# Kernel optimization log

Hardware: AMD Instinct MI355X
Metric: run time of the kernel (lower is better)

## Reference

```python
import jax, jax.numpy as jnp
import numpy as np

EPS = 1e-3    # Keras BatchNormalization default epsilon
ALPHA = 0.3   # Keras LeakyReLU default negative slope


def _bn(x, axes):
    # BatchNormalization(center=False, scale=False) in training mode: batch stats
    m = jnp.mean(x, axis=axes, keepdims=True)
    v = jnp.var(x, axis=axes, keepdims=True)
    return (x - m) * jax.lax.rsqrt(v + EPS)


def _leaky(x):
    return jnp.where(x > 0, x, ALPHA * x)


def setup_inputs() -> dict:
    key = jax.random.key(0)
    ks = jax.random.split(key, 8)
    B, A, D, Hid, H, hd = 8192, 16, 256, 512, 8, 64
    s = 0.02
    return {
        "state": jax.random.normal(ks[0], (B, A, D), jnp.float32),
        "agent_index": 3,
        "Ws": jax.random.normal(ks[1], (D, Hid), jnp.float32) * s,
        "bs": jnp.zeros((Hid,), jnp.float32),
        "Wc": jax.random.normal(ks[2], (D, Hid), jnp.float32) * s,
        "bc": jnp.zeros((Hid,), jnp.float32),
        "Wk": jax.random.normal(ks[3], (H, Hid, hd), jnp.float32) * s,
        "Wq": jax.random.normal(ks[4], (H, Hid, hd), jnp.float32) * s,
        "Wv": jax.random.normal(ks[5], (H, Hid, hd), jnp.float32) * s,
    }


def reference(state, agent_index, Ws, bs, Wc, bc, Wk, Wq, Wv):
    B = state.shape[0]
    H, _, hd = Wk.shape
    ai = int(agent_index)

    # current agent encoder: BN over batch, Dense, LeakyReLU -> [B, Hid]
    cur = state[:, ai, :]
    s_enc = _leaky(_bn(cur, (0,)) @ Ws + bs)

    # other agents encoder: BN over (batch, agent), Dense, LeakyReLU -> [B, A-1, Hid]
    others = jnp.concatenate([state[:, :ai, :], state[:, ai + 1:, :]], axis=1)
    sa_enc = _leaky(_bn(others, (0, 1)) @ Wc + bc)

    # batched per-head projections (replaces the python loop over heads)
    k = jnp.einsum('ban,hnd->bhad', sa_enc, Wk)           # [B,H,A-1,hd]
    v = _leaky(jnp.einsum('ban,hnd->bhad', sa_enc, Wv))   # [B,H,A-1,hd]
    q = jnp.einsum('bn,hnd->bhd', s_enc, Wq)              # [B,H,hd]

    scores = jnp.einsum('bhd,bhad->bha', q, k) / jnp.sqrt(jnp.float32(hd))
    w = jax.nn.softmax(scores, axis=-1)                   # [B,H,A-1]
    att = jnp.einsum('bha,bhad->bhd', w, v)               # [B,H,hd]

    # concat heads in order -> [B, H*hd]
    return att.reshape(B, H * hd)
```

## Files before the change

kernel.cpp:

```cpp
#include <hip/hip_runtime.h>
#include <hip/hip_bf16.h>

typedef __attribute__((ext_vector_type(8))) short short8;
typedef __attribute__((ext_vector_type(8))) unsigned short ushort8;
typedef __attribute__((ext_vector_type(4))) unsigned short bfu4;
typedef __attribute__((ext_vector_type(4))) float f32x4;

__device__ __forceinline__ unsigned short f2bf(float f){
  return __builtin_bit_cast(unsigned short, __float2bfloat16(f));
}
__device__ __forceinline__ float bf2f(unsigned short h){
  unsigned int u = ((unsigned int)h) << 16;
  return __builtin_bit_cast(float, u);
}
__device__ __forceinline__ float leaky(float x){ return x > 0.f ? x : 0.3f * x; }

__global__ __launch_bounds__(1024) void ca_stats_partial(const float* __restrict__ state,
    const int* __restrict__ agp, float* __restrict__ part, int B){
  int q = threadIdx.x & 63, sl = threadIdx.x >> 6;
  int ag = agp[0];
  int bPer = (B + 255) >> 8;
  int b0 = blockIdx.x * bPer;
  f32x4 zero4 = {0.f,0.f,0.f,0.f};
  f32x4 sC = zero4, ssC = zero4, sO = zero4, ssO = zero4;
  for (int b = sl; b < bPer; b += 16){
    int bb = b0 + b;
    if (bb >= B) continue;
    const float* row = state + ((size_t)bb << 12) + q*4;
    #pragma unroll
    for (int a = 0; a < 16; a++){
      f32x4 v = *(const f32x4*)(row + a*256);
      f32x4 vv = v * v;
      if (a == ag){ sC += v; ssC += vv; } else { sO += v; ssO += vv; }
    }
  }
  __shared__ f32x4 red[16][4][64];
  red[sl][0][q] = sC; red[sl][1][q] = ssC; red[sl][2][q] = sO; red[sl][3][q] = ssO;
  __syncthreads();
  if (threadIdx.x < 256){
    int st = threadIdx.x >> 6, qq = threadIdx.x & 63;
    f32x4 s = red[0][st][qq];
    #pragma unroll
    for (int g = 1; g < 16; g++) s += red[g][st][qq];
    *(f32x4*)(part + (size_t)blockIdx.x*1024 + st*256 + qq*4) = s;
  }
}

__global__ __launch_bounds__(1024) void ca_stats_final(const float* __restrict__ part,
    float* __restrict__ stats, int nblk, int B){
  int d = threadIdx.x & 255, sl = threadIdx.x >> 8;
  float sC = 0.f, ssC = 0.f, sO = 0.f, ssO = 0.f;
  for (int g = sl; g < nblk; g += 4){
    const float* p = part + (size_t)g * 1024;
    sC += p[d]; ssC += p[d+256]; sO += p[d+512]; ssO += p[d+768];
  }
  __shared__ float red[4][4][256];
  red[sl][0][d] = sC; red[sl][1][d] = ssC; red[sl][2][d] = sO; red[sl][3][d] = ssO;
  __syncthreads();
  if (sl == 0){
    sC  = red[0][0][d] + red[1][0][d] + red[2][0][d] + red[3][0][d];
    ssC = red[0][1][d] + red[1][1][d] + red[2][1][d] + red[3][1][d];
    sO  = red[0][2][d] + red[1][2][d] + red[2][2][d] + red[3][2][d];
    ssO = red[0][3][d] + red[1][3][d] + red[2][3][d] + red[3][3][d];
    float nC = (float)B, nO = (float)B * 15.f;
    float mC = sC / nC, vC = ssC / nC - mC * mC;
    float mO = sO / nO, vO = ssO / nO - mO * mO;
    float rC = rsqrtf(vC + 1e-3f), rO = rsqrtf(vO + 1e-3f);
    stats[d] = rC; stats[d+256] = mC * rC; stats[d+512] = rO; stats[d+768] = mO * rO;
  }
}

__global__ __launch_bounds__(256) void ca_prep_sc(const float* __restrict__ Ws,
    const float* __restrict__ bs, const float* __restrict__ Wc, const float* __restrict__ bc,
    const float* __restrict__ stats, unsigned short* __restrict__ WsT,
    unsigned short* __restrict__ WcT, unsigned short* __restrict__ WsF,
    unsigned short* __restrict__ WcF, float* __restrict__ bsp, float* __restrict__ bcp,
    int writeT){
  int n = blockIdx.x, d = threadIdx.x;
  float rC = stats[d], mrC = stats[d+256], rO = stats[d+512], mrO = stats[d+768];
  float ws = Ws[(size_t)d*512 + n], wc = Wc[(size_t)d*512 + n];
  unsigned short wsb = f2bf(ws * rC), wcb = f2bf(wc * rO);
  if (writeT){
    WsT[(size_t)n*256 + d] = wsb;
    WcT[(size_t)n*256 + d] = wcb;
  }
  {
    int h = n >> 6, nt = (n >> 4) & 3, j = n & 15;
    int kk = d >> 5, hi = (d >> 3) & 3, e = d & 7;
    size_t fi = (size_t)((h*8 + kk)*4 + nt)*512 + (hi*16 + j)*8 + e;
    WsF[fi] = wsb;
    WcF[fi] = wcb;
  }
  __shared__ float red[256];
  red[d] = mrC * ws;
  __syncthreads();
  for (int s = 128; s > 0; s >>= 1){ if (d < s) red[d] += red[d+s]; __syncthreads(); }
  if (d == 0) bsp[n] = bs[n] - red[0];
  __syncthreads();
  red[d] = mrO * wc;
  __syncthreads();
  for (int s = 128; s > 0; s >>= 1){ if (d < s) red[d] += red[d+s]; __syncthreads(); }
  if (d == 0) bcp[n] = bc[n] - red[0];
}

__global__ __launch_bounds__(512) void ca_prep_kvq(const float* __restrict__ Wk,
    const float* __restrict__ Wv, const float* __restrict__ Wq,
    unsigned short* __restrict__ WkT, unsigned short* __restrict__ WvT,
    unsigned short* __restrict__ WqT, unsigned short* __restrict__ WkF2,
    unsigned short* __restrict__ WvF, unsigned short* __restrict__ WqF, int writeT){
  int c = blockIdx.x & 511, m = blockIdx.x >> 9;
  int n = threadIdx.x;
  if (m == 3){
    size_t idx = (size_t)c*512 + n;
    int h = (int)(idx >> 15), nn = (int)((idx >> 6) & 511), dd = (int)(idx & 63);
    int nt = nn >> 4, j = nn & 15, kq = dd >> 5, hi = (dd >> 3) & 3, e = dd & 7;
    WkF2[(size_t)((h*32 + nt)*2 + kq)*512 + (hi*16 + j)*8 + e] = f2bf(Wk[idx]);
    return;
  }
  if (m == 0 && !writeT) return;
  int h = c >> 6, dd = c & 63;
  const float* W = (m == 0) ? Wk : (m == 1) ? Wv : Wq;
  unsigned short* O = (m == 0) ? WkT : (m == 1) ? WvT : WqT;
  float scale = (m == 2) ? 0.125f : 1.f;
  unsigned short v = f2bf(W[((size_t)h*512 + n)*64 + dd] * scale);
  if (m == 0 || writeT) O[(size_t)c*512 + n] = v;
  if (m != 0){
    int nt = (c >> 4) & 3, j = c & 15;
    int kk = n >> 5, hi = (n >> 3) & 3, e = n & 7;
    size_t fi = (size_t)((h*16 + kk)*4 + nt)*512 + (hi*16 + j)*8 + e;
    if (m == 1) WvF[fi] = v; else WqF[fi] = v;
  }
}

__global__ __launch_bounds__(512) void ca_q_kernel(const float* __restrict__ state,
    const int* __restrict__ agp,
    const unsigned short* __restrict__ WsT, const float* __restrict__ bsp,
    const unsigned short* __restrict__ WqT, unsigned short* __restrict__ Qws){
  __shared__ unsigned short U[32*512];
  __shared__ float bias_s[512];
  unsigned short* Alds = U;
  unsigned short* SE = U;
  int tid = threadIdx.x, lane = tid & 63, w = tid >> 6;
  int j = lane & 15, hi = lane >> 4;
  int b0 = blockIdx.x * 32;
  int ag = agp[0];

  for (int s = tid; s < 32*32; s += 512){
    int row = s >> 5, kg = s & 31;
    const float* p = state + (((size_t)(b0 + row) * 16 + ag) << 8) + kg * 8;
    f32x4 v0 = *(const f32x4*)p, v1 = *(const f32x4*)(p + 4);
    ushort8 hv;
    hv[0]=f2bf(v0[0]); hv[1]=f2bf(v0[1]); hv[2]=f2bf(v0[2]); hv[3]=f2bf(v0[3]);
    hv[4]=f2bf(v1[0]); hv[5]=f2bf(v1[1]); hv[6]=f2bf(v1[2]); hv[7]=f2bf(v1[3]);
    *(ushort8*)&Alds[row*256 + ((kg ^ (row & 7)) << 3)] = hv;
  }
  bias_s[tid & 511] = bsp[tid & 511];
  __syncthreads();

  int cb = w * 64;
  f32x4 zero4 = {0.f, 0.f, 0.f, 0.f};
  f32x4 acc[2][4];
  #pragma unroll
  for (int a1 = 0; a1 < 2; a1++)
    #pragma unroll
    for (int a2 = 0; a2 < 4; a2++) acc[a1][a2] = zero4;

  #pragma unroll
  for (int kk = 0; kk < 8; kk++){
    short8 bfr[4];
    #pragma unroll
    for (int nt = 0; nt < 4; nt++)
      bfr[nt] = *(const short8*)&WsT[(size_t)(cb + nt*16 + j)*256 + kk*32 + hi*8];
    #pragma unroll
    for (int mt = 0; mt < 2; mt++){
      int row = mt*16 + j;
      short8 afr = *(const short8*)&Alds[row*256 + ((((kk << 2) | hi) ^ (row & 7)) << 3)];
      #pragma unroll
      for (int nt = 0; nt < 4; nt++)
        acc[mt][nt] = __builtin_amdgcn_mfma_f32_16x16x32_bf16(afr, bfr[nt], acc[mt][nt], 0, 0, 0);
    }
  }
  __syncthreads();
  #pragma unroll
  for (int mt = 0; mt < 2; mt++)
    #pragma unroll
    for (int nt = 0; nt < 4; nt++)
      #pragma unroll
      for (int i = 0; i < 4; i++){
        int row = mt*16 + hi*4 + i, col = cb + nt*16 + j;
        float x = leaky(acc[mt][nt][i] + bias_s[col]);
        SE[row*512 + ((((col >> 3) ^ (row & 7)) << 3) | (col & 7))] = f2bf(x);
      }
  __syncthreads();

  f32x4 qa[2][4];
  #pragma unroll
  for (int a1 = 0; a1 < 2; a1++)
    #pragma unroll
    for (int a2 = 0; a2 < 4; a2++) qa[a1][a2] = zero4;
  #pragma unroll
  for (int kk = 0; kk < 16; kk++){
    short8 bfr[4];
    #pragma unroll
    for (int nt = 0; nt < 4; nt++)
      bfr[nt] = *(const short8*)&WqT[(size_t)(cb + nt*16 + j)*512 + kk*32 + hi*8];
    #pragma unroll
    for (int mt = 0; mt < 2; mt++){
      int row = mt*16 + j;
      short8 afr = *(const short8*)&SE[row*512 + ((((kk << 2) | hi) ^ (row & 7)) << 3)];
      #pragma unroll
      for (int nt = 0; nt < 4; nt++)
        qa[mt][nt] = __builtin_amdgcn_mfma_f32_16x16x32_bf16(afr, bfr[nt], qa[mt][nt], 0, 0, 0);
    }
  }
  #pragma unroll
  for (int mt = 0; mt < 2; mt++)
    #pragma unroll
    for (int nt = 0; nt < 4; nt++)
      #pragma unroll
      for (int i = 0; i < 4; i++)
        Qws[(size_t)(b0 + mt*16 + hi*4 + i)*512 + cb + nt*16 + j] = f2bf(qa[mt][nt][i]);
}

__global__ __launch_bounds__(512) void ca_q_kernel_qk(const float* __restrict__ state,
    const int* __restrict__ agp,
    const unsigned short* __restrict__ WsF, const float* __restrict__ bsp,
    const unsigned short* __restrict__ WqF, const unsigned short* __restrict__ WkF2,
    unsigned short* __restrict__ QKws){
  __shared__ unsigned short U[16*512];
  __shared__ float bias_s[512];
  unsigned short* Alds = U;
  unsigned short* SE = U;
  unsigned short* Qlds = U;
  int tid = threadIdx.x, lane = tid & 63, w = tid >> 6;
  int j = lane & 15, hi = lane >> 4;
  int b0 = blockIdx.x * 16;
  int ag = agp[0];
  f32x4 zero4 = {0.f, 0.f, 0.f, 0.f};

  {
    int row = tid >> 5, kg = tid & 31;
    const float* p = state + (((size_t)(b0 + row) * 16 + ag) << 8) + kg * 8;
    f32x4 v0 = *(const f32x4*)p, v1 = *(const f32x4*)(p + 4);
    ushort8 hv;
    hv[0]=f2bf(v0[0]); hv[1]=f2bf(v0[1]); hv[2]=f2bf(v0[2]); hv[3]=f2bf(v0[3]);
    hv[4]=f2bf(v1[0]); hv[5]=f2bf(v1[1]); hv[6]=f2bf(v1[2]); hv[7]=f2bf(v1[3]);
    *(ushort8*)&Alds[row*256 + ((kg ^ (row & 7)) << 3)] = hv;
  }
  bias_s[tid] = bsp[tid];
  __syncthreads();

  int cb = w * 64;

  f32x4 acc[4];
  #pragma unroll
  for (int a2 = 0; a2 < 4; a2++) acc[a2] = zero4;
  #pragma unroll
  for (int kk = 0; kk < 8; kk++){
    short8 bfr[4];
    #pragma unroll
    for (int nt = 0; nt < 4; nt++)
      bfr[nt] = *(const short8*)&WsF[(size_t)((w*8 + kk)*4 + nt)*512 + lane*8];
    short8 afr = *(const short8*)&Alds[j*256 + ((((kk << 2) | hi) ^ (j & 7)) << 3)];
    #pragma unroll
    for (int nt = 0; nt < 4; nt++)
      acc[nt] = __builtin_amdgcn_mfma_f32_16x16x32_bf16(bfr[nt], afr, acc[nt], 0, 0, 0);
  }
  __syncthreads();
  #pragma unroll
  for (int nt = 0; nt < 4; nt++){
    int nb = cb + nt*16 + hi*4;
    int g = nb >> 3;
    bfu4 pk;
    #pragma unroll
    for (int i = 0; i < 4; i++) pk[i] = f2bf(leaky(acc[nt][i] + bias_s[nb + i]));
    *(bfu4*)&SE[j*512 + ((g ^ (j & 7)) << 3) + (hi & 1)*4] = pk;
  }
  __syncthreads();

  f32x4 qa[4];
  #pragma unroll
  for (int a2 = 0; a2 < 4; a2++) qa[a2] = zero4;
  #pragma unroll
  for (int kk = 0; kk < 16; kk++){
    short8 bfr[4];
    #pragma unroll
    for (int nt = 0; nt < 4; nt++)
      bfr[nt] = *(const short8*)&WqF[(size_t)((w*16 + kk)*4 + nt)*512 + lane*8];
    short8 afr = *(const short8*)&SE[j*512 + ((((kk << 2) | hi) ^ (j & 7)) << 3)];
    #pragma unroll
    for (int nt = 0; nt < 4; nt++)
      qa[nt] = __builtin_amdgcn_mfma_f32_16x16x32_bf16(bfr[nt], afr, qa[nt], 0, 0, 0);
  }
  __syncthreads();
  #pragma unroll
  for (int nt = 0; nt < 4; nt++){
    int nb = cb + nt*16 + hi*4;
    int g = nb >> 3;
    bfu4 pk;
    #pragma unroll
    for (int i = 0; i < 4; i++) pk[i] = f2bf(qa[nt][i]);
    *(bfu4*)&Qlds[j*512 + ((g ^ (j & 7)) << 3) + (hi & 1)*4] = pk;
  }
  __syncthreads();

  short8 aq[2];
  #pragma unroll
  for (int kq = 0; kq < 2; kq++){
    int gq = w*8 + kq*4 + hi;
    aq[kq] = *(const short8*)&Qlds[j*512 + ((gq ^ (j & 7)) << 3)];
  }
  for (int nt = 0; nt < 32; nt++){
    short8 bf0 = *(const short8*)&WkF2[(size_t)((w*32 + nt)*2 + 0)*512 + lane*8];
    short8 bf1 = *(const short8*)&WkF2[(size_t)((w*32 + nt)*2 + 1)*512 + lane*8];
    f32x4 qt = zero4;
    qt = __builtin_amdgcn_mfma_f32_16x16x32_bf16(bf0, aq[0], qt, 0, 0, 0);
    qt = __builtin_amdgcn_mfma_f32_16x16x32_bf16(bf1, aq[1], qt, 0, 0, 0);
    bfu4 pk;
    pk[0] = f2bf(qt[0]); pk[1] = f2bf(qt[1]); pk[2] = f2bf(qt[2]); pk[3] = f2bf(qt[3]);
    *(bfu4*)&QKws[((size_t)(b0 + j)*8 + w)*512 + nt*16 + hi*4] = pk;
  }
}

__global__ __launch_bounds__(512) void ca_main_kernel_qk(const float* __restrict__ state,
    const int* __restrict__ agp,
    const unsigned short* __restrict__ WcF, const float* __restrict__ bcp,
    const unsigned short* __restrict__ WvF, const unsigned short* __restrict__ QKws,
    float* __restrict__ out){
  __shared__ unsigned short U[128*512];
  __shared__ float bias_s[512];
  __shared__ float Wl[8*16*8];
  unsigned short* Alds = U;
  unsigned short* SA = U;
  int tid = threadIdx.x, lane = tid & 63, w = tid >> 6;
  int j = lane & 15, hi = lane >> 4;
  int b0 = blockIdx.x * 8;
  int ag = agp[0];
  f32x4 zero4 = {0.f, 0.f, 0.f, 0.f};
  short8 zero8 = {0,0,0,0,0,0,0,0};

  #pragma unroll
  for (int g = 0; g < 2; g++){
    f32x4 st0[4], st1[4];
    #pragma unroll
    for (int it = 0; it < 4; it++){
      int s = tid + 512*(g*4 + it);
      int row = s >> 5, kg = s & 31;
      int bl = row >> 4, ai = row & 15;
      if (ai < 15){
        int a = ai + (ai >= ag ? 1 : 0);
        const float* p = state + (((size_t)(b0 + bl) * 16 + a) << 8) + kg * 8;
        st0[it] = *(const f32x4*)p;
        st1[it] = *(const f32x4*)(p + 4);
      } else { st0[it] = zero4; st1[it] = zero4; }
    }
    #pragma unroll
    for (int it = 0; it < 4; it++){
      int s = tid + 512*(g*4 + it);
      int row = s >> 5, kg = s & 31;
      ushort8 hv;
      hv[0]=f2bf(st0[it][0]); hv[1]=f2bf(st0[it][1]); hv[2]=f2bf(st0[it][2]); hv[3]=f2bf(st0[it][3]);
      hv[4]=f2bf(st1[it][0]); hv[5]=f2bf(st1[it][1]); hv[6]=f2bf(st1[it][2]); hv[7]=f2bf(st1[it][3]);
      *(ushort8*)&Alds[row*256 + ((kg ^ (row & 7)) << 3)] = hv;
    }
  }
  bias_s[tid] = bcp[tid];
  __syncthreads();

  int cb = w * 64;

  f32x4 acc[8][4];
  #pragma unroll
  for (int a1 = 0; a1 < 8; a1++)
    #pragma unroll
    for (int a2 = 0; a2 < 4; a2++) acc[a1][a2] = zero4;
  {
    short8 bcur[4], bnxt[4];
    #pragma unroll
    for (int nt = 0; nt < 4; nt++)
      bcur[nt] = *(const short8*)&WcF[(size_t)((w*8 + 0)*4 + nt)*512 + lane*8];
    #pragma unroll 1
    for (int kk = 0; kk < 8; kk++){
      if (kk < 7){
        #pragma unroll
        for (int nt = 0; nt < 4; nt++)
          bnxt[nt] = *(const short8*)&WcF[(size_t)((w*8 + kk + 1)*4 + nt)*512 + lane*8];
      }
      #pragma unroll
      for (int mt = 0; mt < 8; mt++){
        int row = mt*16 + j;
        short8 afr = *(const short8*)&Alds[row*256 + ((((kk << 2) | hi) ^ (row & 7)) << 3)];
        #pragma unroll
        for (int nt = 0; nt < 4; nt++)
          acc[mt][nt] = __builtin_amdgcn_mfma_f32_16x16x32_bf16(bcur[nt], afr, acc[mt][nt], 0, 0, 0);
      }
      #pragma unroll
      for (int nt = 0; nt < 4; nt++) bcur[nt] = bnxt[nt];
    }
  }
  __syncthreads();
  #pragma unroll
  for (int mt = 0; mt < 8; mt++)
    #pragma unroll
    for (int nt = 0; nt < 4; nt++){
      int m = mt*16 + j;
      int nb = cb + nt*16 + hi*4;
      int g = nb >> 3;
      bfu4 pk;
      #pragma unroll
      for (int i = 0; i < 4; i++) pk[i] = f2bf(leaky(acc[mt][nt][i] + bias_s[nb + i]));
      *(bfu4*)&SA[m*512 + ((g ^ (m & 7)) << 3) + (hi & 1)*4] = pk;
    }
  __syncthreads();

  f32x4 qs = zero4;
  {
    size_t qbase = ((size_t)(b0 + w)*8 + (j & 7))*512;
    #pragma unroll
    for (int kk = 0; kk < 16; kk++){
      short8 bq = *(const short8*)&QKws[qbase + kk*32 + hi*8];
      if (j >= 8) bq = zero8;
      int row = w*16 + j;
      short8 afr = *(const short8*)&SA[row*512 + ((((kk << 2) | hi) ^ (row & 7)) << 3)];
      qs = __builtin_amdgcn_mfma_f32_16x16x32_bf16(afr, bq, qs, 0, 0, 0);
    }
  }
  {
    float sv0 = qs[0], sv1 = qs[1], sv2 = qs[2], sv3 = qs[3];
    sv3 = (hi == 3) ? -1e30f : sv3;
    float m = fmaxf(fmaxf(sv0, sv1), fmaxf(sv2, sv3));
    m = fmaxf(m, __shfl_xor(m, 16)); m = fmaxf(m, __shfl_xor(m, 32));
    float e0 = __expf(sv0-m), e1 = __expf(sv1-m), e2 = __expf(sv2-m), e3 = __expf(sv3-m);
    float sum = e0 + e1 + e2 + e3;
    sum += __shfl_xor(sum, 16); sum += __shfl_xor(sum, 32);
    float inv = 1.f / sum;
    if (j < 8){
      Wl[w*128 + (hi*4+0)*8 + j] = e0*inv;
      Wl[w*128 + (hi*4+1)*8 + j] = e1*inv;
      Wl[w*128 + (hi*4+2)*8 + j] = e2*inv;
      Wl[w*128 + (hi*4+3)*8 + j] = e3*inv;
    }
  }

  f32x4 va[8][4];
  #pragma unroll
  for (int a1 = 0; a1 < 8; a1++)
    #pragma unroll
    for (int a2 = 0; a2 < 4; a2++) va[a1][a2] = zero4;
  {
    short8 bcur[4], bnxt[4];
    #pragma unroll
    for (int nt = 0; nt < 4; nt++)
      bcur[nt] = *(const short8*)&WvF[(size_t)((w*16 + 0)*4 + nt)*512 + lane*8];
    #pragma unroll 1
    for (int kk = 0; kk < 16; kk++){
      if (kk < 15){
        #pragma unroll
        for (int nt = 0; nt < 4; nt++)
          bnxt[nt] = *(const short8*)&WvF[(size_t)((w*16 + kk + 1)*4 + nt)*512 + lane*8];
      }
      #pragma unroll
      for (int mt = 0; mt < 8; mt++){
        int row = mt*16 + j;
        short8 afr = *(const short8*)&SA[row*512 + ((((kk << 2) | hi) ^ (row & 7)) << 3)];
        #pragma unroll
        for (int nt = 0; nt < 4; nt++)
          va[mt][nt] = __builtin_amdgcn_mfma_f32_16x16x32_bf16(afr, bcur[nt], va[mt][nt], 0, 0, 0);
      }
      #pragma unroll
      for (int nt = 0; nt < 4; nt++) bcur[nt] = bnxt[nt];
    }
  }
  __syncthreads();

  #pragma unroll
  for (int mt = 0; mt < 8; mt++){
    float w0 = Wl[mt*128 + (hi*4+0)*8 + w];
    float w1 = Wl[mt*128 + (hi*4+1)*8 + w];
    float w2 = Wl[mt*128 + (hi*4+2)*8 + w];
    float w3 = Wl[mt*128 + (hi*4+3)*8 + w];
    float ap0 = w0*leaky(va[mt][0][0]) + w1*leaky(va[mt][0][1]) + w2*leaky(va[mt][0][2]) + w3*leaky(va[mt][0][3]);
    float ap1 = w0*leaky(va[mt][1][0]) + w1*leaky(va[mt][1][1]) + w2*leaky(va[mt][1][2]) + w3*leaky(va[mt][1][3]);
    float ap2 = w0*leaky(va[mt][2][0]) + w1*leaky(va[mt][2][1]) + w2*leaky(va[mt][2][2]) + w3*leaky(va[mt][2][3]);
    float ap3 = w0*leaky(va[mt][3][0]) + w1*leaky(va[mt][3][1]) + w2*leaky(va[mt][3][2]) + w3*leaky(va[mt][3][3]);
    ap0 += __shfl_xor(ap0, 16); ap0 += __shfl_xor(ap0, 32);
    ap1 += __shfl_xor(ap1, 16); ap1 += __shfl_xor(ap1, 32);
    ap2 += __shfl_xor(ap2, 16); ap2 += __shfl_xor(ap2, 32);
    ap3 += __shfl_xor(ap3, 16); ap3 += __shfl_xor(ap3, 32);
    float val = (hi == 0) ? ap0 : (hi == 1) ? ap1 : (hi == 2) ? ap2 : ap3;
    out[(size_t)(b0 + mt)*512 + cb + lane] = val;
  }
}

__global__ __launch_bounds__(512) void ca_main_kernel(const float* __restrict__ state,
    const int* __restrict__ agp,
    const unsigned short* __restrict__ WcT, const float* __restrict__ bcp,
    const unsigned short* __restrict__ WkT, const unsigned short* __restrict__ WvT,
    const unsigned short* __restrict__ Qws, float* __restrict__ out){
  __shared__ unsigned short U[128*512];
  __shared__ unsigned short Qs[8*512];
  __shared__ float bias_s[512];
  unsigned short* Alds = U;
  unsigned short* SA = U;
  int tid = threadIdx.x, lane = tid & 63, w = tid >> 6;
  int j = lane & 15, hi = lane >> 4;
  int b0 = blockIdx.x * 8;
  int ag = agp[0];
  f32x4 zero4 = {0.f, 0.f, 0.f, 0.f};

  #pragma unroll
  for (int g = 0; g < 2; g++){
    f32x4 st0[4], st1[4];
    #pragma unroll
    for (int it = 0; it < 4; it++){
      int s = tid + 512*(g*4 + it);
      int row = s >> 5, kg = s & 31;
      int bl = row >> 4, ai = row & 15;
      if (ai < 15){
        int a = ai + (ai >= ag ? 1 : 0);
        const float* p = state + (((size_t)(b0 + bl) * 16 + a) << 8) + kg * 8;
        st0[it] = *(const f32x4*)p;
        st1[it] = *(const f32x4*)(p + 4);
      } else { st0[it] = zero4; st1[it] = zero4; }
    }
    #pragma unroll
    for (int it = 0; it < 4; it++){
      int s = tid + 512*(g*4 + it);
      int row = s >> 5, kg = s & 31;
      ushort8 hv;
      hv[0]=f2bf(st0[it][0]); hv[1]=f2bf(st0[it][1]); hv[2]=f2bf(st0[it][2]); hv[3]=f2bf(st0[it][3]);
      hv[4]=f2bf(st1[it][0]); hv[5]=f2bf(st1[it][1]); hv[6]=f2bf(st1[it][2]); hv[7]=f2bf(st1[it][3]);
      *(ushort8*)&Alds[row*256 + ((kg ^ (row & 7)) << 3)] = hv;
    }
  }
  *(ushort8*)&Qs[tid*8] = *(const ushort8*)&Qws[(size_t)b0*512 + tid*8];
  bias_s[tid] = bcp[tid];
  __syncthreads();

  int cb = w * 64;

  f32x4 acc[8][4];
  #pragma unroll
  for (int a1 = 0; a1 < 8; a1++)
    #pragma unroll
    for (int a2 = 0; a2 < 4; a2++) acc[a1][a2] = zero4;
  {
    short8 bcur[4], bnxt[4];
    #pragma unroll
    for (int nt = 0; nt < 4; nt++)
      bcur[nt] = *(const short8*)&WcT[(size_t)(cb + nt*16 + j)*256 + hi*8];
    #pragma unroll 1
    for (int kk = 0; kk < 8; kk++){
      if (kk < 7){
        #pragma unroll
        for (int nt = 0; nt < 4; nt++)
          bnxt[nt] = *(const short8*)&WcT[(size_t)(cb + nt*16 + j)*256 + (kk+1)*32 + hi*8];
      }
      #pragma unroll
      for (int mt = 0; mt < 8; mt++){
        int row = mt*16 + j;
        short8 afr = *(const short8*)&Alds[row*256 + ((((kk << 2) | hi) ^ (row & 7)) << 3)];
        #pragma unroll
        for (int nt = 0; nt < 4; nt++)
          acc[mt][nt] = __builtin_amdgcn_mfma_f32_16x16x32_bf16(afr, bcur[nt], acc[mt][nt], 0, 0, 0);
      }
      #pragma unroll
      for (int nt = 0; nt < 4; nt++) bcur[nt] = bnxt[nt];
    }
  }
  __syncthreads();
  #pragma unroll
  for (int mt = 0; mt < 8; mt++)
    #pragma unroll
    for (int nt = 0; nt < 4; nt++)
      #pragma unroll
      for (int i = 0; i < 4; i++){
        int row = mt*16 + hi*4 + i, col = cb + nt*16 + j;
        float x = leaky(acc[mt][nt][i] + bias_s[col]);
        SA[row*512 + ((((col >> 3) ^ (row & 7)) << 3) | (col & 7))] = f2bf(x);
      }
  __syncthreads();

  f32x4 ka[8][4];
  #pragma unroll
  for (int a1 = 0; a1 < 8; a1++)
    #pragma unroll
    for (int a2 = 0; a2 < 4; a2++) ka[a1][a2] = zero4;
  {
    short8 bcur[4], bnxt[4];
    #pragma unroll
    for (int nt = 0; nt < 4; nt++)
      bcur[nt] = *(const short8*)&WkT[(size_t)(cb + nt*16 + j)*512 + hi*8];
    #pragma unroll 1
    for (int kk = 0; kk < 16; kk++){
      if (kk < 15){
        #pragma unroll
        for (int nt = 0; nt < 4; nt++)
          bnxt[nt] = *(const short8*)&WkT[(size_t)(cb + nt*16 + j)*512 + (kk+1)*32 + hi*8];
      }
      #pragma unroll
      for (int mt = 0; mt < 8; mt++){
        int row = mt*16 + j;
        short8 afr = *(const short8*)&SA[row*512 + ((((kk << 2) | hi) ^ (row & 7)) << 3)];
        #pragma unroll
        for (int nt = 0; nt < 4; nt++)
          ka[mt][nt] = __builtin_amdgcn_mfma_f32_16x16x32_bf16(afr, bcur[nt], ka[mt][nt], 0, 0, 0);
      }
      #pragma unroll
      for (int nt = 0; nt < 4; nt++) bcur[nt] = bnxt[nt];
    }
  }

  float wgt[8][4];
  #pragma unroll
  for (int mt = 0; mt < 8; mt++){
    float sv[4];
    #pragma unroll
    for (int i = 0; i < 4; i++){
      float t = 0.f;
      #pragma unroll
      for (int nt = 0; nt < 4; nt++)
        t += bf2f(Qs[mt*512 + cb + nt*16 + j]) * ka[mt][nt][i];
      t += __shfl_xor(t, 1); t += __shfl_xor(t, 2);
      t += __shfl_xor(t, 4); t += __shfl_xor(t, 8);
      sv[i] = t;
    }
    sv[3] = (hi == 3) ? -1e30f : sv[3];
    float m = fmaxf(fmaxf(sv[0], sv[1]), fmaxf(sv[2], sv[3]));
    m = fmaxf(m, __shfl_xor(m, 16)); m = fmaxf(m, __shfl_xor(m, 32));
    float e0 = __expf(sv[0]-m), e1 = __expf(sv[1]-m), e2 = __expf(sv[2]-m), e3 = __expf(sv[3]-m);
    float sum = e0 + e1 + e2 + e3;
    sum += __shfl_xor(sum, 16); sum += __shfl_xor(sum, 32);
    float inv = 1.f / sum;
    wgt[mt][0] = e0*inv; wgt[mt][1] = e1*inv; wgt[mt][2] = e2*inv; wgt[mt][3] = e3*inv;
  }

  f32x4 va[8][4];
  #pragma unroll
  for (int a1 = 0; a1 < 8; a1++)
    #pragma unroll
    for (int a2 = 0; a2 < 4; a2++) va[a1][a2] = zero4;
  {
    short8 bcur[4], bnxt[4];
    #pragma unroll
    for (int nt = 0; nt < 4; nt++)
      bcur[nt] = *(const short8*)&WvT[(size_t)(cb + nt*16 + j)*512 + hi*8];
    #pragma unroll 1
    for (int kk = 0; kk < 16; kk++){
      if (kk < 15){
        #pragma unroll
        for (int nt = 0; nt < 4; nt++)
          bnxt[nt] = *(const short8*)&WvT[(size_t)(cb + nt*16 + j)*512 + (kk+1)*32 + hi*8];
      }
      #pragma unroll
      for (int mt = 0; mt < 8; mt++){
        int row = mt*16 + j;
        short8 afr = *(const short8*)&SA[row*512 + ((((kk << 2) | hi) ^ (row & 7)) << 3)];
        #pragma unroll
        for (int nt = 0; nt < 4; nt++)
          va[mt][nt] = __builtin_amdgcn_mfma_f32_16x16x32_bf16(afr, bcur[nt], va[mt][nt], 0, 0, 0);
      }
      #pragma unroll
      for (int nt = 0; nt < 4; nt++) bcur[nt] = bnxt[nt];
    }
  }

  #pragma unroll
  for (int mt = 0; mt < 8; mt++){
    float ap0 = 0.f, ap1 = 0.f, ap2 = 0.f, ap3 = 0.f;
    #pragma unroll
    for (int i = 0; i < 4; i++){
      float wv = wgt[mt][i];
      ap0 += wv * leaky(va[mt][0][i]);
      ap1 += wv * leaky(va[mt][1][i]);
      ap2 += wv * leaky(va[mt][2][i]);
      ap3 += wv * leaky(va[mt][3][i]);
    }
    ap0 += __shfl_xor(ap0, 16); ap0 += __shfl_xor(ap0, 32);
    ap1 += __shfl_xor(ap1, 16); ap1 += __shfl_xor(ap1, 32);
    ap2 += __shfl_xor(ap2, 16); ap2 += __shfl_xor(ap2, 32);
    ap3 += __shfl_xor(ap3, 16); ap3 += __shfl_xor(ap3, 32);
    float val = (hi == 0) ? ap0 : (hi == 1) ? ap1 : (hi == 2) ? ap2 : ap3;
    out[(size_t)(b0 + mt)*512 + cb + lane] = val;
  }
}

extern "C" void kernel_launch(void* const* d_in, const int* in_sizes, int n_in,
                              void* d_out, int out_size, void* d_ws, size_t ws_size,
                              hipStream_t stream) {
  const float* state = (const float*)d_in[0];
  const int*   agp   = (const int*)d_in[1];
  const float* Ws    = (const float*)d_in[2];
  const float* bs    = (const float*)d_in[3];
  const float* Wc    = (const float*)d_in[4];
  const float* bc    = (const float*)d_in[5];
  const float* Wk    = (const float*)d_in[6];
  const float* Wq    = (const float*)d_in[7];
  const float* Wv    = (const float*)d_in[8];
  float* out = (float*)d_out;
  int B = in_sizes[0] / 4096;

  char* wsb = (char*)d_ws;
  float* part  = (float*)wsb;
  float* stats = (float*)(wsb + (1 << 20));
  float* bsp   = (float*)(wsb + (1 << 20) + 4096);
  float* bcp   = (float*)(wsb + (1 << 20) + 6144);
  unsigned short* WsT  = (unsigned short*)(wsb + (1 << 20) + 8192);
  unsigned short* WcT  = WsT  + 512*256;
  unsigned short* WkT  = WcT  + 512*256;
  unsigned short* WvT  = WkT  + 512*512;
  unsigned short* WqT  = WvT  + 512*512;
  unsigned short* WkF2 = WqT  + 512*512;
  unsigned short* Qws  = WkF2 + 512*512;
  unsigned short* QKws = Qws  + (size_t)B*512;
  unsigned short* WsF  = Qws;
  unsigned short* WcF  = WsF + 512*256;
  unsigned short* WqF  = WcF + 512*256;
  unsigned short* WvF  = WqF + 512*512;

  size_t need = ((size_t)(1 << 20) + 8192)
              + 2ull*(512*256 + 512*256 + 512*512 + 512*512 + 512*512 + 512*512)
              + 2ull*B*512 + 2ull*B*8*512;
  bool qkp = (ws_size >= need);
  int writeT = qkp ? 0 : 1;

  hipLaunchKernelGGL(ca_stats_partial, dim3(256), dim3(1024), 0, stream, state, agp, part, B);
  hipLaunchKernelGGL(ca_stats_final,   dim3(1),   dim3(1024), 0, stream, part, stats, 256, B);
  hipLaunchKernelGGL(ca_prep_sc,       dim3(512), dim3(256), 0, stream, Ws, bs, Wc, bc, stats, WsT, WcT, WsF, WcF, bsp, bcp, writeT);
  hipLaunchKernelGGL(ca_prep_kvq,      dim3(2048),dim3(512), 0, stream, Wk, Wv, Wq, WkT, WvT, WqT, WkF2, WvF, WqF, writeT);
  if (qkp){
    hipLaunchKernelGGL(ca_q_kernel_qk,   dim3(B/16),dim3(512), 0, stream, state, agp, WsF, bsp, WqF, WkF2, QKws);
    hipLaunchKernelGGL(ca_main_kernel_qk,dim3(B/8), dim3(512), 0, stream, state, agp, WcF, bcp, WvF, QKws, out);
  } else {
    hipLaunchKernelGGL(ca_q_kernel,      dim3(B/32),dim3(512), 0, stream, state, agp, WsT, bsp, WqT, Qws);
    hipLaunchKernelGGL(ca_main_kernel,   dim3(B/8), dim3(512), 0, stream, state, agp, WcT, bcp, WkT, WvT, Qws, out);
  }
}
```

Baseline: 235.6 us.

## Fuse query/QK projection into main attention kernel and parallelize stats finalization

Removes the separate ca_q_kernel_qk launch and computes the current-agent encoding, Q projection and Q·Wk products inside ca_main_kernel_qk for each block's 8 batch rows. Rows are padded to 16 with zeros, so half the MFMA work in that phase is wasted. It also splits ca_stats_final across 4 blocks of 64 features each instead of one block. This saves a launch and the inter-kernel gap, but adds LDS usage and per-block work to the main kernel, which may lower occupancy. The QKws round trip through global memory remains.

```diff
diff --git a/kernel.cpp b/kernel.cpp
--- a/kernel.cpp
+++ b/kernel.cpp
@@ -48,20 +48,22 @@
 
 __global__ __launch_bounds__(1024) void ca_stats_final(const float* __restrict__ part,
     float* __restrict__ stats, int nblk, int B){
-  int d = threadIdx.x & 255, sl = threadIdx.x >> 8;
+  int dl = threadIdx.x & 63, sl = threadIdx.x >> 6;
+  int d = blockIdx.x*64 + dl;
   float sC = 0.f, ssC = 0.f, sO = 0.f, ssO = 0.f;
-  for (int g = sl; g < nblk; g += 4){
+  for (int g = sl; g < nblk; g += 16){
     const float* p = part + (size_t)g * 1024;
     sC += p[d]; ssC += p[d+256]; sO += p[d+512]; ssO += p[d+768];
   }
-  __shared__ float red[4][4][256];
-  red[sl][0][d] = sC; red[sl][1][d] = ssC; red[sl][2][d] = sO; red[sl][3][d] = ssO;
+  __shared__ float red[16][4][64];
+  red[sl][0][dl] = sC; red[sl][1][dl] = ssC; red[sl][2][dl] = sO; red[sl][3][dl] = ssO;
   __syncthreads();
   if (sl == 0){
-    sC  = red[0][0][d] + red[1][0][d] + red[2][0][d] + red[3][0][d];
-    ssC = red[0][1][d] + red[1][1][d] + red[2][1][d] + red[3][1][d];
-    sO  = red[0][2][d] + red[1][2][d] + red[2][2][d] + red[3][2][d];
-    ssO = red[0][3][d] + red[1][3][d] + red[2][3][d] + red[3][3][d];
+    sC = 0.f; ssC = 0.f; sO = 0.f; ssO = 0.f;
+    #pragma unroll
+    for (int g = 0; g < 16; g++){
+      sC += red[g][0][dl]; ssC += red[g][1][dl]; sO += red[g][2][dl]; ssO += red[g][3][dl];
+    }
     float nC = (float)B, nO = (float)B * 15.f;
     float mC = sC / nC, vC = ssC / nC - mC * mC;
     float mO = sO / nO, vO = ssO / nO - mO * mO;
@@ -222,116 +224,21 @@
         Qws[(size_t)(b0 + mt*16 + hi*4 + i)*512 + cb + nt*16 + j] = f2bf(qa[mt][nt][i]);
 }
 
-__global__ __launch_bounds__(512) void ca_q_kernel_qk(const float* __restrict__ state,
-    const int* __restrict__ agp,
-    const unsigned short* __restrict__ WsF, const float* __restrict__ bsp,
-    const unsigned short* __restrict__ WqF, const unsigned short* __restrict__ WkF2,
-    unsigned short* __restrict__ QKws){
-  __shared__ unsigned short U[16*512];
-  __shared__ float bias_s[512];
-  unsigned short* Alds = U;
-  unsigned short* SE = U;
-  unsigned short* Qlds = U;
-  int tid = threadIdx.x, lane = tid & 63, w = tid >> 6;
-  int j = lane & 15, hi = lane >> 4;
-  int b0 = blockIdx.x * 16;
-  int ag = agp[0];
-  f32x4 zero4 = {0.f, 0.f, 0.f, 0.f};
-
-  {
-    int row = tid >> 5, kg = tid & 31;
-    const float* p = state + (((size_t)(b0 + row) * 16 + ag) << 8) + kg * 8;
-    f32x4 v0 = *(const f32x4*)p, v1 = *(const f32x4*)(p + 4);
-    ushort8 hv;
-    hv[0]=f2bf(v0[0]); hv[1]=f2bf(v0[1]); hv[2]=f2bf(v0[2]); hv[3]=f2bf(v0[3]);
-    hv[4]=f2bf(v1[0]); hv[5]=f2bf(v1[1]); hv[6]=f2bf(v1[2]); hv[7]=f2bf(v1[3]);
-    *(ushort8*)&Alds[row*256 + ((kg ^ (row & 7)) << 3)] = hv;
-  }
-  bias_s[tid] = bsp[tid];
-  __syncthreads();
-
-  int cb = w * 64;
-
-  f32x4 acc[4];
-  #pragma unroll
-  for (int a2 = 0; a2 < 4; a2++) acc[a2] = zero4;
-  #pragma unroll
-  for (int kk = 0; kk < 8; kk++){
-    short8 bfr[4];
-    #pragma unroll
-    for (int nt = 0; nt < 4; nt++)
-      bfr[nt] = *(const short8*)&WsF[(size_t)((w*8 + kk)*4 + nt)*512 + lane*8];
-    short8 afr = *(const short8*)&Alds[j*256 + ((((kk << 2) | hi) ^ (j & 7)) << 3)];
-    #pragma unroll
-    for (int nt = 0; nt < 4; nt++)
-      acc[nt] = __builtin_amdgcn_mfma_f32_16x16x32_bf16(bfr[nt], afr, acc[nt], 0, 0, 0);
-  }
-  __syncthreads();
-  #pragma unroll
-  for (int nt = 0; nt < 4; nt++){
-    int nb = cb + nt*16 + hi*4;
-    int g = nb >> 3;
-    bfu4 pk;
-    #pragma unroll
-    for (int i = 0; i < 4; i++) pk[i] = f2bf(leaky(acc[nt][i] + bias_s[nb + i]));
-    *(bfu4*)&SE[j*512 + ((g ^ (j & 7)) << 3) + (hi & 1)*4] = pk;
-  }
-  __syncthreads();
-
-  f32x4 qa[4];
-  #pragma unroll
-  for (int a2 = 0; a2 < 4; a2++) qa[a2] = zero4;
-  #pragma unroll
-  for (int kk = 0; kk < 16; kk++){
-    short8 bfr[4];
-    #pragma unroll
-    for (int nt = 0; nt < 4; nt++)
-      bfr[nt] = *(const short8*)&WqF[(size_t)((w*16 + kk)*4 + nt)*512 + lane*8];
-    short8 afr = *(const short8*)&SE[j*512 + ((((kk << 2) | hi) ^ (j & 7)) << 3)];
-    #pragma unroll
-    for (int nt = 0; nt < 4; nt++)
-      qa[nt] = __builtin_amdgcn_mfma_f32_16x16x32_bf16(bfr[nt], afr, qa[nt], 0, 0, 0);
-  }
-  __syncthreads();
-  #pragma unroll
-  for (int nt = 0; nt < 4; nt++){
-    int nb = cb + nt*16 + hi*4;
-    int g = nb >> 3;
-    bfu4 pk;
-    #pragma unroll
-    for (int i = 0; i < 4; i++) pk[i] = f2bf(qa[nt][i]);
-    *(bfu4*)&Qlds[j*512 + ((g ^ (j & 7)) << 3) + (hi & 1)*4] = pk;
-  }
-  __syncthreads();
-
-  short8 aq[2];
-  #pragma unroll
-  for (int kq = 0; kq < 2; kq++){
-    int gq = w*8 + kq*4 + hi;
-    aq[kq] = *(const short8*)&Qlds[j*512 + ((gq ^ (j & 7)) << 3)];
-  }
-  for (int nt = 0; nt < 32; nt++){
-    short8 bf0 = *(const short8*)&WkF2[(size_t)((w*32 + nt)*2 + 0)*512 + lane*8];
-    short8 bf1 = *(const short8*)&WkF2[(size_t)((w*32 + nt)*2 + 1)*512 + lane*8];
-    f32x4 qt = zero4;
-    qt = __builtin_amdgcn_mfma_f32_16x16x32_bf16(bf0, aq[0], qt, 0, 0, 0);
-    qt = __builtin_amdgcn_mfma_f32_16x16x32_bf16(bf1, aq[1], qt, 0, 0, 0);
-    bfu4 pk;
-    pk[0] = f2bf(qt[0]); pk[1] = f2bf(qt[1]); pk[2] = f2bf(qt[2]); pk[3] = f2bf(qt[3]);
-    *(bfu4*)&QKws[((size_t)(b0 + j)*8 + w)*512 + nt*16 + hi*4] = pk;
-  }
-}
-
 __global__ __launch_bounds__(512) void ca_main_kernel_qk(const float* __restrict__ state,
     const int* __restrict__ agp,
     const unsigned short* __restrict__ WcF, const float* __restrict__ bcp,
-    const unsigned short* __restrict__ WvF, const unsigned short* __restrict__ QKws,
+    const unsigned short* __restrict__ WsF, const float* __restrict__ bsp,
+    const unsigned short* __restrict__ WqF, const unsigned short* __restrict__ WkF2,
+    const unsigned short* __restrict__ WvF, unsigned short* __restrict__ QKws,
     float* __restrict__ out){
   __shared__ unsigned short U[128*512];
-  __shared__ float bias_s[512];
+  __shared__ unsigned short SEq[16*512];
+  __shared__ float bias_c[512];
+  __shared__ float bias_q[512];
   __shared__ float Wl[8*16*8];
   unsigned short* Alds = U;
   unsigned short* SA = U;
+  unsigned short* CURlds = U + 32768;
   int tid = threadIdx.x, lane = tid & 63, w = tid >> 6;
   int j = lane & 15, hi = lane >> 4;
   int b0 = blockIdx.x * 8;
@@ -364,10 +271,99 @@
       *(ushort8*)&Alds[row*256 + ((kg ^ (row & 7)) << 3)] = hv;
     }
   }
-  bias_s[tid] = bcp[tid];
+  {
+    int row = tid >> 5, kg = tid & 31;
+    ushort8 hv = {0,0,0,0,0,0,0,0};
+    if (row < 8){
+      const float* p = state + (((size_t)(b0 + row) * 16 + ag) << 8) + kg * 8;
+      f32x4 v0 = *(const f32x4*)p, v1 = *(const f32x4*)(p + 4);
+      hv[0]=f2bf(v0[0]); hv[1]=f2bf(v0[1]); hv[2]=f2bf(v0[2]); hv[3]=f2bf(v0[3]);
+      hv[4]=f2bf(v1[0]); hv[5]=f2bf(v1[1]); hv[6]=f2bf(v1[2]); hv[7]=f2bf(v1[3]);
+    }
+    *(ushort8*)&CURlds[row*256 + ((kg ^ (row & 7)) << 3)] = hv;
+  }
+  bias_c[tid] = bcp[tid];
+  bias_q[tid] = bsp[tid];
   __syncthreads();
 
   int cb = w * 64;
+
+  {
+    f32x4 acc[4];
+    #pragma unroll
+    for (int a2 = 0; a2 < 4; a2++) acc[a2] = zero4;
+    #pragma unroll
+    for (int kk = 0; kk < 8; kk++){
+      short8 bfr[4];
+      #pragma unroll
+      for (int nt = 0; nt < 4; nt++)
+        bfr[nt] = *(const short8*)&WsF[(size_t)((w*8 + kk)*4 + nt)*512 + lane*8];
+      short8 afr = *(const short8*)&CURlds[j*256 + ((((kk << 2) | hi) ^ (j & 7)) << 3)];
+      #pragma unroll
+      for (int nt = 0; nt < 4; nt++)
+        acc[nt] = __builtin_amdgcn_mfma_f32_16x16x32_bf16(bfr[nt], afr, acc[nt], 0, 0, 0);
+    }
+    __syncthreads();
+    #pragma unroll
+    for (int nt = 0; nt < 4; nt++){
+      int nb = cb + nt*16 + hi*4;
+      int g = nb >> 3;
+      bfu4 pk;
+      #pragma unroll
+      for (int i = 0; i < 4; i++) pk[i] = f2bf(leaky(acc[nt][i] + bias_q[nb + i]));
+      *(bfu4*)&SEq[j*512 + ((g ^ (j & 7)) << 3) + (hi & 1)*4] = pk;
+    }
+    __syncthreads();
+  }
+
+  {
+    f32x4 qa[4];
+    #pragma unroll
+    for (int a2 = 0; a2 < 4; a2++) qa[a2] = zero4;
+    #pragma unroll
+    for (int kk = 0; kk < 16; kk++){
+      short8 bfr[4];
+      #pragma unroll
+      for (int nt = 0; nt < 4; nt++)
+        bfr[nt] = *(const short8*)&WqF[(size_t)((w*16 + kk)*4 + nt)*512 + lane*8];
+      short8 afr = *(const short8*)&SEq[j*512 + ((((kk << 2) | hi) ^ (j & 7)) << 3)];
+      #pragma unroll
+      for (int nt = 0; nt < 4; nt++)
+        qa[nt] = __builtin_amdgcn_mfma_f32_16x16x32_bf16(bfr[nt], afr, qa[nt], 0, 0, 0);
+    }
+    __syncthreads();
+    #pragma unroll
+    for (int nt = 0; nt < 4; nt++){
+      int nb = cb + nt*16 + hi*4;
+      int g = nb >> 3;
+      bfu4 pk;
+      #pragma unroll
+      for (int i = 0; i < 4; i++) pk[i] = f2bf(qa[nt][i]);
+      *(bfu4*)&SEq[j*512 + ((g ^ (j & 7)) << 3) + (hi & 1)*4] = pk;
+    }
+    __syncthreads();
+  }
+
+  {
+    short8 aq[2];
+    #pragma unroll
+    for (int kq = 0; kq < 2; kq++){
+      int gq = w*8 + kq*4 + hi;
+      aq[kq] = *(const short8*)&SEq[j*512 + ((gq ^ (j & 7)) << 3)];
+    }
+    for (int nt = 0; nt < 32; nt++){
+      short8 bf0 = *(const short8*)&WkF2[(size_t)((w*32 + nt)*2 + 0)*512 + lane*8];
+      short8 bf1 = *(const short8*)&WkF2[(size_t)((w*32 + nt)*2 + 1)*512 + lane*8];
+      f32x4 qt = zero4;
+      qt = __builtin_amdgcn_mfma_f32_16x16x32_bf16(bf0, aq[0], qt, 0, 0, 0);
+      qt = __builtin_amdgcn_mfma_f32_16x16x32_bf16(bf1, aq[1], qt, 0, 0, 0);
+      if (j < 8){
+        bfu4 pk;
+        pk[0] = f2bf(qt[0]); pk[1] = f2bf(qt[1]); pk[2] = f2bf(qt[2]); pk[3] = f2bf(qt[3]);
+        *(bfu4*)&QKws[((size_t)(b0 + j)*8 + w)*512 + nt*16 + hi*4] = pk;
+      }
+    }
+  }
 
   f32x4 acc[8][4];
   #pragma unroll
@@ -408,7 +404,7 @@
       int g = nb >> 3;
       bfu4 pk;
       #pragma unroll
-      for (int i = 0; i < 4; i++) pk[i] = f2bf(leaky(acc[mt][nt][i] + bias_s[nb + i]));
+      for (int i = 0; i < 4; i++) pk[i] = f2bf(leaky(acc[mt][nt][i] + bias_c[nb + i]));
       *(bfu4*)&SA[m*512 + ((g ^ (m & 7)) << 3) + (hi & 1)*4] = pk;
     }
   __syncthreads();
@@ -725,12 +721,12 @@
   int writeT = qkp ? 0 : 1;
 
   hipLaunchKernelGGL(ca_stats_partial, dim3(256), dim3(1024), 0, stream, state, agp, part, B);
-  hipLaunchKernelGGL(ca_stats_final,   dim3(1),   dim3(1024), 0, stream, part, stats, 256, B);
+  hipLaunchKernelGGL(ca_stats_final,   dim3(4),   dim3(1024), 0, stream, part, stats, 256, B);
   hipLaunchKernelGGL(ca_prep_sc,       dim3(512), dim3(256), 0, stream, Ws, bs, Wc, bc, stats, WsT, WcT, WsF, WcF, bsp, bcp, writeT);
   hipLaunchKernelGGL(ca_prep_kvq,      dim3(2048),dim3(512), 0, stream, Wk, Wv, Wq, WkT, WvT, WqT, WkF2, WvF, WqF, writeT);
   if (qkp){
-    hipLaunchKernelGGL(ca_q_kernel_qk,   dim3(B/16),dim3(512), 0, stream, state, agp, WsF, bsp, WqF, WkF2, QKws);
-    hipLaunchKernelGGL(ca_main_kernel_qk,dim3(B/8), dim3(512), 0, stream, state, agp, WcF, bcp, WvF, QKws, out);
+    hipLaunchKernelGGL(ca_main_kernel_qk, dim3(B/8), dim3(512), 0, stream, state, agp,
+                       WcF, bcp, WsF, bsp, WqF, WkF2, WvF, QKws, out);
   } else {
     hipLaunchKernelGGL(ca_q_kernel,      dim3(B/32),dim3(512), 0, stream, state, agp, WsT, bsp, WqT, Qws);
     hipLaunchKernelGGL(ca_main_kernel,   dim3(B/8), dim3(512), 0, stream, state, agp, WcT, bcp, WkT, WvT, Qws, out);
```

Measured after the change: 255.5 us. 1.08x slower.
